# Optimization experiments

Hardware: AMD Instinct MI355X
Metric: run time of the kernel (lower is better)

Reference implementation:

```python
import jax, jax.numpy as jnp
import numpy as np

B, S, H, NH = 8, 1024, 1024, 4
D = H // NH
NEG = jnp.float32(-2**32 + 1)


def setup_inputs() -> dict:
    key = jax.random.key(0)
    ks = jax.random.split(key, 12)
    w = 1.0 / np.sqrt(H)
    wf = 1.0 / np.sqrt(2 * H)
    return {
        "memory": jax.random.normal(ks[0], (B, S, H), jnp.float32),
        "decoder_input": jax.random.normal(ks[1], (B, S, H), jnp.float32),
        "mask": jax.random.bernoulli(ks[2], 0.2, (B, S, S)),
        "query_mask": (jax.random.uniform(ks[3], (B, S)) > 0.1).astype(jnp.float32),
        "Wk": jax.random.normal(ks[4], (H, H), jnp.float32) * w,
        "Wv": jax.random.normal(ks[5], (H, H), jnp.float32) * w,
        "Wq": jax.random.normal(ks[6], (H, H), jnp.float32) * w,
        "Wf": jax.random.normal(ks[7], (2 * H, H), jnp.float32) * wf,
        "bf": jnp.zeros((H,), jnp.float32),
        "gamma": jnp.ones((H,), jnp.float32),
        "beta": jnp.zeros((H,), jnp.float32),
        "g_factor": jax.random.uniform(ks[8], (1,), jnp.float32, 1e4, 2e4),
    }


def reference(memory, decoder_input, mask, query_mask, Wk, Wv, Wq, Wf, bf, gamma, beta, g_factor):
    b, sq, hdim = decoder_input.shape
    sk = memory.shape[1]

    def heads(x, W, s):  # -> (NH, B, s, D), matching torch permute(2,0,1,3)
        return (x @ W).reshape(b, s, NH, D).transpose(2, 0, 1, 3)

    k = heads(memory, Wk, sk)
    v = heads(memory, Wv, sk)
    q = heads(decoder_input, Wq, sq)

    attn = jnp.einsum("hbqd,hbkd->hbqk", q, k) / jnp.sqrt(jnp.float32(D))
    idx = jnp.arange(sk, dtype=jnp.float32)
    gauss = (idx[:, None] - idx[None, :]) ** 2 / g_factor[0]  # (sq, sk), sq==sk
    attn = attn - gauss
    attn = jnp.where(mask[None], NEG, attn)
    attn = jax.nn.softmax(attn, axis=-1)
    attn = attn * query_mask[None, :, :, None]  # post-softmax query mask

    res = jnp.einsum("hbqk,hbkd->hbqd", attn, v)
    res = res.transpose(1, 2, 0, 3).reshape(b, sq, hdim)

    out = jnp.concatenate([decoder_input, res], axis=-1) @ Wf + bf
    out = out + decoder_input
    mu = out.mean(-1, keepdims=True)
    var = ((out - mu) ** 2).mean(-1, keepdims=True)
    out = (out - mu) / jnp.sqrt(var + 1e-5) * gamma + beta
    return out, attn.reshape(NH * b, sq, sk)
```

## Files before the change

### kernel.cpp

```cpp
#include <hip/hip_runtime.h>

#define B_ 8
#define S_ 1024
#define H_ 1024
#define NH_ 4
#define D_ 256
#define M_ 8192

typedef unsigned int u32;
typedef unsigned short u16;
typedef __attribute__((ext_vector_type(4))) float f32x4;
typedef __attribute__((ext_vector_type(8))) short s16x8;

__device__ __forceinline__ float bf2f(u16 b) { return __uint_as_float(((u32)b) << 16); }
__device__ __forceinline__ u16 f2bf(float f) {
    u32 x = __float_as_uint(f);
    return (u16)((x + 0x7fffu + ((x >> 16) & 1u)) >> 16);
}

__global__ void init_flags_k(int* fl) { fl[0] = 0; fl[1] = 0; fl[2] = 0; }

__global__ __launch_bounds__(256) void or_mask_k(const u32* __restrict__ m, int* __restrict__ fl) {
    u32 v = m[blockIdx.x * 256 + threadIdx.x];
#pragma unroll
    for (int o = 32; o; o >>= 1) v |= __shfl_xor(v, o, 64);
    if ((threadIdx.x & 63) == 0) atomicOr(fl + 1, (int)v);
}

__global__ void classify_mask_k(int* fl) {
    u32 R = (u32)fl[1];
    int c;
    if (R == 0x3F803F80u)      c = 2;
    else if (R == 0x3F800000u) c = 3;
    else if (R & 0xFFFFFF00u)  c = 0;
    else                       c = 1;
    fl[2] = c;
}

__global__ __launch_bounds__(256) void tcast_k(const float* __restrict__ src, u16* __restrict__ dst,
                                               int R, int C) {
    __shared__ float sb[32][33];
    const int c0 = blockIdx.x * 32, r0 = blockIdx.y * 32;
    const int tx = threadIdx.x & 31, ty = threadIdx.x >> 5;
#pragma unroll
    for (int i = 0; i < 4; i++)
        sb[ty + 8 * i][tx] = src[(size_t)(r0 + ty + 8 * i) * C + c0 + tx];
    __syncthreads();
#pragma unroll
    for (int i = 0; i < 4; i++)
        dst[(size_t)(c0 + ty + 8 * i) * R + r0 + tx] = f2bf(sb[tx][ty + 8 * i]);
}

__global__ __launch_bounds__(256) void castbf_k(const float* __restrict__ src, u16* __restrict__ dst) {
    const int i = blockIdx.x * 256 + threadIdx.x;
    float4 v = ((const float4*)src)[i];
    ushort4 o;
    o.x = f2bf(v.x); o.y = f2bf(v.y); o.z = f2bf(v.z); o.w = f2bf(v.w);
    ((ushort4*)dst)[i] = o;
}

template<int AMODE>
__device__ __forceinline__ void gemm_core(
    const float* __restrict__ A32, const u16* __restrict__ A16, int lda,
    const u16* __restrict__ Bp, int ldb, int K, int m0, int n0,
    short* As, short* Bs, f32x4 acc[4][4])
{
    const int t = threadIdx.x;
    const int lane = t & 63, wave = t >> 6;
    const int wy = wave >> 1, wx = wave & 1;
    const int mq = lane >> 4, ml = lane & 15;
    const int srow = t >> 2, skq = t & 3;

    for (int k0 = 0; k0 < K; k0 += 32) {
        __syncthreads();
#pragma unroll
        for (int it = 0; it < 2; it++) {
            const int row = srow + it * 64;
            const int kk = k0 + skq * 8;
            short* dst = As + row * 40 + skq * 8;
            if (AMODE == 0) {
                const float* s = A32 + (size_t)(m0 + row) * lda + kk;
                float4 v0 = *(const float4*)s, v1 = *(const float4*)(s + 4);
                s16x8 p;
                p[0] = (short)f2bf(v0.x); p[1] = (short)f2bf(v0.y);
                p[2] = (short)f2bf(v0.z); p[3] = (short)f2bf(v0.w);
                p[4] = (short)f2bf(v1.x); p[5] = (short)f2bf(v1.y);
                p[6] = (short)f2bf(v1.z); p[7] = (short)f2bf(v1.w);
                *(s16x8*)dst = p;
            } else if (AMODE == 1) {
                *(s16x8*)dst = *(const s16x8*)(A16 + (size_t)(m0 + row) * lda + kk);
            } else {
                if (kk < 1024) {
                    const float* s = A32 + (size_t)(m0 + row) * 1024 + kk;
                    float4 v0 = *(const float4*)s, v1 = *(const float4*)(s + 4);
                    s16x8 p;
                    p[0] = (short)f2bf(v0.x); p[1] = (short)f2bf(v0.y);
                    p[2] = (short)f2bf(v0.z); p[3] = (short)f2bf(v0.w);
                    p[4] = (short)f2bf(v1.x); p[5] = (short)f2bf(v1.y);
                    p[6] = (short)f2bf(v1.z); p[7] = (short)f2bf(v1.w);
                    *(s16x8*)dst = p;
                } else {
                    *(s16x8*)dst = *(const s16x8*)(A16 + (size_t)(m0 + row) * 1024 + (kk - 1024));
                }
            }
        }
#pragma unroll
        for (int it = 0; it < 2; it++) {
            const int row = srow + it * 64;
            *(s16x8*)(Bs + row * 40 + skq * 8) =
                *(const s16x8*)(Bp + (size_t)(n0 + row) * ldb + k0 + skq * 8);
        }
        __syncthreads();
        s16x8 af[4], bfr[4];
#pragma unroll
        for (int i = 0; i < 4; i++) {
            af[i]  = *(s16x8*)(As + (wy * 64 + i * 16 + ml) * 40 + mq * 8);
            bfr[i] = *(s16x8*)(Bs + (wx * 64 + i * 16 + ml) * 40 + mq * 8);
        }
#pragma unroll
        for (int mi = 0; mi < 4; mi++)
#pragma unroll
            for (int ni = 0; ni < 4; ni++)
                acc[mi][ni] = __builtin_amdgcn_mfma_f32_16x16x32_bf16(af[mi], bfr[ni], acc[mi][ni], 0, 0, 0);
    }
}

__global__ __launch_bounds__(256) void gemm_proj_k(const u16* __restrict__ A, const u16* __restrict__ WT,
                                                   u16* __restrict__ C) {
    __shared__ short As[128 * 40];
    __shared__ short Bs[128 * 40];
    const int m0 = blockIdx.y * 128, n0 = blockIdx.x * 128;
    f32x4 acc[4][4];
#pragma unroll
    for (int i = 0; i < 4; i++)
#pragma unroll
        for (int j = 0; j < 4; j++) acc[i][j] = 0;
    gemm_core<1>(nullptr, A, H_, WT, H_, H_, m0, n0, As, Bs, acc);
    const int lane = threadIdx.x & 63, wave = threadIdx.x >> 6;
    const int wy = wave >> 1, wx = wave & 1, mq = lane >> 4, ml = lane & 15;
#pragma unroll
    for (int mi = 0; mi < 4; mi++)
#pragma unroll
        for (int ni = 0; ni < 4; ni++) {
            const int n = n0 + wx * 64 + ni * 16 + ml;
#pragma unroll
            for (int r = 0; r < 4; r++) {
                const int m = m0 + wy * 64 + mi * 16 + mq * 4 + r;
                C[(size_t)m * H_ + n] = f2bf(acc[mi][ni][r]);
            }
        }
}

__global__ __launch_bounds__(256) void gemm_vt_k(const u16* __restrict__ A, const u16* __restrict__ WT,
                                                 u16* __restrict__ VT) {
    __shared__ short As[128 * 40];
    __shared__ short Bs[128 * 40];
    const int m0 = blockIdx.y * 128, n0 = blockIdx.x * 128;
    f32x4 acc[4][4];
#pragma unroll
    for (int i = 0; i < 4; i++)
#pragma unroll
        for (int j = 0; j < 4; j++) acc[i][j] = 0;
    gemm_core<1>(nullptr, A, H_, WT, H_, H_, m0, n0, As, Bs, acc);
    const int lane = threadIdx.x & 63, wave = threadIdx.x >> 6;
    const int wy = wave >> 1, wx = wave & 1, mq = lane >> 4, ml = lane & 15;
#pragma unroll
    for (int mi = 0; mi < 4; mi++)
#pragma unroll
        for (int ni = 0; ni < 4; ni++) {
            const int n = n0 + wx * 64 + ni * 16 + ml;
            const int mbase = m0 + wy * 64 + mi * 16 + mq * 4;
            const int b = mbase >> 10, s = mbase & 1023;
            ushort4 w;
            w.x = f2bf(acc[mi][ni][0]); w.y = f2bf(acc[mi][ni][1]);
            w.z = f2bf(acc[mi][ni][2]); w.w = f2bf(acc[mi][ni][3]);
            *(ushort4*)(VT + ((size_t)(b * 1024 + n)) * 1024 + s) = w;
        }
}

__global__ __launch_bounds__(512, 2) void qk_sm_k(
    const u16* __restrict__ Qb, const u16* __restrict__ Kb,
    const void* __restrict__ mask, const float* __restrict__ gfac,
    const int* __restrict__ fl, const float* __restrict__ qmask,
    float* __restrict__ attn)
{
    __shared__ short Bs[1024 * 40];
    __shared__ short As[64 * 40];
    __shared__ float red[2][32][4];

    const int flat = blockIdx.x;
    const int wgid = (flat & 7) * 64 + (flat >> 3);
    const int z = wgid >> 4, m0 = (wgid & 15) * 64;
    const int h = z >> 3, b = z & 7;

    const u16* Aq = Qb + (size_t)b * S_ * H_ + h * D_;
    const u16* Bk = Kb + (size_t)b * S_ * H_ + h * D_;

    const int t = threadIdx.x;
    const int lane = t & 63, wave = t >> 6;
    const int wm = wave >> 2, wn = wave & 3;
    const int mq = lane >> 4, ml = lane & 15;

    f32x4 acc[2][16];
#pragma unroll
    for (int mi = 0; mi < 2; mi++)
#pragma unroll
        for (int nf = 0; nf < 16; nf++) acc[mi][nf] = 0;

    for (int k0 = 0; k0 < D_; k0 += 32) {
        __syncthreads();
        if (t < 256) {
            const int row = t >> 2, kq = t & 3;
            *(s16x8*)(As + row * 40 + kq * 8) =
                *(const s16x8*)(Aq + (size_t)(m0 + row) * H_ + k0 + kq * 8);
        }
#pragma unroll
        for (int it = 0; it < 8; it++) {
            const int c = it * 512 + t;
            const int row = c >> 2, kq = c & 3;
            *(s16x8*)(Bs + row * 40 + kq * 8) =
                *(const s16x8*)(Bk + (size_t)row * H_ + k0 + kq * 8);
        }
        __syncthreads();
        s16x8 af0 = *(s16x8*)(As + (wm * 32 + ml) * 40 + mq * 8);
        s16x8 af1 = *(s16x8*)(As + (wm * 32 + 16 + ml) * 40 + mq * 8);
#pragma unroll
        for (int g4 = 0; g4 < 4; g4++) {
            s16x8 bf4[4];
#pragma unroll
            for (int j = 0; j < 4; j++)
                bf4[j] = *(s16x8*)(Bs + (wn * 256 + (g4 * 4 + j) * 16 + ml) * 40 + mq * 8);
#pragma unroll
            for (int j = 0; j < 4; j++) {
                acc[0][g4 * 4 + j] = __builtin_amdgcn_mfma_f32_16x16x32_bf16(af0, bf4[j], acc[0][g4 * 4 + j], 0, 0, 0);
                acc[1][g4 * 4 + j] = __builtin_amdgcn_mfma_f32_16x16x32_bf16(af1, bf4[j], acc[1][g4 * 4 + j], 0, 0, 0);
            }
        }
    }

    const float ginv = 1.0f / gfac[0];
    const int code = fl[2];
    const size_t zrow = (size_t)z * S_;
    float rmax[2][4], rsum[2][4], scv[2][4];

#pragma unroll
    for (int mi = 0; mi < 2; mi++)
#pragma unroll
        for (int r = 0; r < 4; r++) {
            const int qg = m0 + wm * 32 + mi * 16 + mq * 4 + r;
            const size_t mbase = ((size_t)b * S_ + qg) * S_;
            float mx = -3.0e38f;
#pragma unroll
            for (int nf = 0; nf < 16; nf++) {
                const int kg = wn * 256 + nf * 16 + ml;
                float diff = (float)(qg - kg);
                float val = acc[mi][nf][r] * 0.0625f - diff * diff * ginv;
                int mv;
                if (code == 0)      mv = ((const unsigned char*)mask)[mbase + kg];
                else if (code == 1) mv = ((const int*)mask)[mbase + kg];
                else if (code == 2) mv = (((const u16*)mask)[mbase + kg] != 0);
                else                mv = (((const u32*)mask)[mbase + kg] != 0);
                if (mv) val = -4294967296.0f;
                acc[mi][nf][r] = val;
                mx = fmaxf(mx, val);
            }
            rmax[mi][r] = mx;
        }
#pragma unroll
    for (int o = 1; o < 16; o <<= 1)
#pragma unroll
        for (int mi = 0; mi < 2; mi++)
#pragma unroll
            for (int r = 0; r < 4; r++)
                rmax[mi][r] = fmaxf(rmax[mi][r], __shfl_xor(rmax[mi][r], o, 64));
    if (ml == 0)
#pragma unroll
        for (int mi = 0; mi < 2; mi++)
#pragma unroll
            for (int r = 0; r < 4; r++) red[wm][mi * 16 + mq * 4 + r][wn] = rmax[mi][r];
    __syncthreads();
#pragma unroll
    for (int mi = 0; mi < 2; mi++)
#pragma unroll
        for (int r = 0; r < 4; r++) {
            const int rr = mi * 16 + mq * 4 + r;
            rmax[mi][r] = fmaxf(fmaxf(red[wm][rr][0], red[wm][rr][1]),
                                fmaxf(red[wm][rr][2], red[wm][rr][3]));
        }
    __syncthreads();
#pragma unroll
    for (int mi = 0; mi < 2; mi++)
#pragma unroll
        for (int r = 0; r < 4; r++) {
            float s = 0.f;
#pragma unroll
            for (int nf = 0; nf < 16; nf++) {
                float p = __expf(acc[mi][nf][r] - rmax[mi][r]);
                acc[mi][nf][r] = p;
                s += p;
            }
            rsum[mi][r] = s;
        }
#pragma unroll
    for (int o = 1; o < 16; o <<= 1)
#pragma unroll
        for (int mi = 0; mi < 2; mi++)
#pragma unroll
            for (int r = 0; r < 4; r++) rsum[mi][r] += __shfl_xor(rsum[mi][r], o, 64);
    if (ml == 0)
#pragma unroll
        for (int mi = 0; mi < 2; mi++)
#pragma unroll
            for (int r = 0; r < 4; r++) red[wm][mi * 16 + mq * 4 + r][wn] = rsum[mi][r];
    __syncthreads();
#pragma unroll
    for (int mi = 0; mi < 2; mi++)
#pragma unroll
        for (int r = 0; r < 4; r++) {
            const int rr = mi * 16 + mq * 4 + r;
            const int qg = m0 + wm * 32 + mi * 16 + mq * 4 + r;
            const float s = red[wm][rr][0] + red[wm][rr][1] + red[wm][rr][2] + red[wm][rr][3];
            scv[mi][r] = qmask[b * S_ + qg] / s;
        }
#pragma unroll
    for (int mi = 0; mi < 2; mi++)
#pragma unroll
        for (int r = 0; r < 4; r++) {
            const int qg = m0 + wm * 32 + mi * 16 + mq * 4 + r;
            float* prow = attn + (zrow + qg) * S_ + wn * 256 + ml;
            const float sc = scv[mi][r];
#pragma unroll
            for (int nf = 0; nf < 16; nf++)
                prow[nf * 16] = acc[mi][nf][r] * sc;
        }
}

__global__ __launch_bounds__(256) void pv_mfma_k(const float* __restrict__ attnF, const u16* __restrict__ VT,
                                                 u16* __restrict__ resB) {
    __shared__ short As[128 * 40];
    __shared__ short Bs[128 * 40];
    const int z = blockIdx.z, h = z >> 3, b = z & 7;
    const float* Ap = attnF + (size_t)z * S_ * S_;
    const u16* Bp = VT + ((size_t)(b * 1024 + h * D_)) * 1024;
    const int m0 = blockIdx.y * 128, n0 = blockIdx.x * 128;
    f32x4 acc[4][4];
#pragma unroll
    for (int i = 0; i < 4; i++)
#pragma unroll
        for (int j = 0; j < 4; j++) acc[i][j] = 0;
    gemm_core<0>(Ap, nullptr, S_, Bp, 1024, S_, m0, n0, As, Bs, acc);
    u16* C = resB + (size_t)b * S_ * H_ + h * D_;
    const int lane = threadIdx.x & 63, wave = threadIdx.x >> 6;
    const int wy = wave >> 1, wx = wave & 1, mq = lane >> 4, ml = lane & 15;
#pragma unroll
    for (int mi = 0; mi < 4; mi++)
#pragma unroll
        for (int ni = 0; ni < 4; ni++) {
            const int n = n0 + wx * 64 + ni * 16 + ml;
#pragma unroll
            for (int r = 0; r < 4; r++) {
                const int m = m0 + wy * 64 + mi * 16 + mq * 4 + r;
                C[(size_t)m * H_ + n] = f2bf(acc[mi][ni][r]);
            }
        }
}

__global__ __launch_bounds__(256) void final_mfma_k(const float* __restrict__ dec, const u16* __restrict__ resB,
                                                    const u16* __restrict__ WfT, const float* __restrict__ bfv,
                                                    u16* __restrict__ tmp) {
    __shared__ short As[128 * 40];
    __shared__ short Bs[128 * 40];
    const int m0 = blockIdx.y * 128, n0 = blockIdx.x * 128;
    f32x4 acc[4][4];
#pragma unroll
    for (int i = 0; i < 4; i++)
#pragma unroll
        for (int j = 0; j < 4; j++) acc[i][j] = 0;
    gemm_core<2>(dec, resB, H_, WfT, 2048, 2048, m0, n0, As, Bs, acc);
    const int lane = threadIdx.x & 63, wave = threadIdx.x >> 6;
    const int wy = wave >> 1, wx = wave & 1, mq = lane >> 4, ml = lane & 15;
#pragma unroll
    for (int mi = 0; mi < 4; mi++)
#pragma unroll
        for (int ni = 0; ni < 4; ni++) {
            const int n = n0 + wx * 64 + ni * 16 + ml;
#pragma unroll
            for (int r = 0; r < 4; r++) {
                const int m = m0 + wy * 64 + mi * 16 + mq * 4 + r;
                float val = acc[mi][ni][r] + bfv[n] + dec[(size_t)m * H_ + n];
                tmp[(size_t)m * H_ + n] = f2bf(val);
            }
        }
}

__global__ __launch_bounds__(256) void ln2_k(const u16* __restrict__ tmp, const float* __restrict__ gm,
                                             const float* __restrict__ bt, float* __restrict__ out) {
    const int m = blockIdx.x, t = threadIdx.x;
    ushort4 u = ((const ushort4*)(tmp + (size_t)m * H_))[t];
    float xa[4] = {bf2f(u.x), bf2f(u.y), bf2f(u.z), bf2f(u.w)};
    float s = 0.f, s2 = 0.f;
#pragma unroll
    for (int i = 0; i < 4; i++) { s += xa[i]; s2 += xa[i] * xa[i]; }
#pragma unroll
    for (int o = 32; o; o >>= 1) { s += __shfl_xor(s, o, 64); s2 += __shfl_xor(s2, o, 64); }
    __shared__ float rs[4], rs2[4];
    if ((t & 63) == 0) { rs[t >> 6] = s; rs2[t >> 6] = s2; }
    __syncthreads();
    s  = rs[0] + rs[1] + rs[2] + rs[3];
    s2 = rs2[0] + rs2[1] + rs2[2] + rs2[3];
    float mu = s * (1.f / 1024.f);
    float var = s2 * (1.f / 1024.f) - mu * mu;
    float rstd = rsqrtf(var + 1e-5f);
    float ov[4];
#pragma unroll
    for (int i = 0; i < 4; i++) {
        int n = t * 4 + i;
        ov[i] = (xa[i] - mu) * rstd * gm[n] + bt[n];
    }
    *(float4*)(out + (size_t)m * H_ + t * 4) = make_float4(ov[0], ov[1], ov[2], ov[3]);
}

extern "C" void kernel_launch(void* const* d_in, const int* in_sizes, int n_in,
                              void* d_out, int out_size, void* d_ws, size_t ws_size,
                              hipStream_t stream) {
    const float* memory = (const float*)d_in[0];
    const float* dec    = (const float*)d_in[1];
    const void*  mask   = d_in[2];
    const float* qmask  = (const float*)d_in[3];
    const float* Wk     = (const float*)d_in[4];
    const float* Wv     = (const float*)d_in[5];
    const float* Wq     = (const float*)d_in[6];
    const float* Wf     = (const float*)d_in[7];
    const float* bfv    = (const float*)d_in[8];
    const float* gamma  = (const float*)d_in[9];
    const float* beta   = (const float*)d_in[10];
    const float* gfac   = (const float*)d_in[11];

    char* ws = (char*)d_ws;
    int* fl  = (int*)ws;
    u16* WqT = (u16*)(ws + (1u  << 20));
    u16* WkT = (u16*)(ws + (3u  << 20));
    u16* WvT = (u16*)(ws + (5u  << 20));
    u16* WfT = (u16*)(ws + (7u  << 20));
    u16* Qb  = (u16*)(ws + (11u << 20));
    u16* Kb  = (u16*)(ws + (27u << 20));
    u16* VT  = (u16*)(ws + (43u << 20));
    u16* resB = Kb;
    u16* tmpB = Qb;

    float* out   = (float*)d_out;
    float* attnF = out + (size_t)B_ * S_ * H_;

    u16* memB = (u16*)attnF;
    u16* decB = memB + (size_t)B_ * S_ * H_;

    init_flags_k<<<1, 1, 0, stream>>>(fl);
    or_mask_k<<<256, 256, 0, stream>>>((const u32*)mask, fl);
    classify_mask_k<<<1, 1, 0, stream>>>(fl);

    tcast_k<<<dim3(32, 32), 256, 0, stream>>>(Wq, WqT, 1024, 1024);
    tcast_k<<<dim3(32, 32), 256, 0, stream>>>(Wk, WkT, 1024, 1024);
    tcast_k<<<dim3(32, 32), 256, 0, stream>>>(Wv, WvT, 1024, 1024);
    tcast_k<<<dim3(32, 64), 256, 0, stream>>>(Wf, WfT, 2048, 1024);

    castbf_k<<<8192, 256, 0, stream>>>(memory, memB);
    castbf_k<<<8192, 256, 0, stream>>>(dec,    decB);

    gemm_proj_k<<<dim3(8, 64), 256, 0, stream>>>(decB, WqT, Qb);
    gemm_proj_k<<<dim3(8, 64), 256, 0, stream>>>(memB, WkT, Kb);
    gemm_vt_k  <<<dim3(8, 64), 256, 0, stream>>>(memB, WvT, VT);

    qk_sm_k<<<512, 512, 0, stream>>>(Qb, Kb, mask, gfac, fl, qmask, attnF);
    pv_mfma_k<<<dim3(2, 8, 32), 256, 0, stream>>>(attnF, VT, resB);
    final_mfma_k<<<dim3(8, 64), 256, 0, stream>>>(dec, resB, WfT, bfv, tmpB);
    ln2_k<<<M_, 256, 0, stream>>>(tmpB, gamma, beta, out);
}
```

Measured before the change: 634.2 us.

## Fuse PV matmul into QK-softmax kernel using bf16 probabilities in LDS

After: 616.7 us. 2.8% less time.

```diff
diff --git a/kernel.cpp b/kernel.cpp
--- a/kernel.cpp
+++ b/kernel.cpp
@@ -78,16 +78,7 @@
             const int row = srow + it * 64;
             const int kk = k0 + skq * 8;
             short* dst = As + row * 40 + skq * 8;
-            if (AMODE == 0) {
-                const float* s = A32 + (size_t)(m0 + row) * lda + kk;
-                float4 v0 = *(const float4*)s, v1 = *(const float4*)(s + 4);
-                s16x8 p;
-                p[0] = (short)f2bf(v0.x); p[1] = (short)f2bf(v0.y);
-                p[2] = (short)f2bf(v0.z); p[3] = (short)f2bf(v0.w);
-                p[4] = (short)f2bf(v1.x); p[5] = (short)f2bf(v1.y);
-                p[6] = (short)f2bf(v1.z); p[7] = (short)f2bf(v1.w);
-                *(s16x8*)dst = p;
-            } else if (AMODE == 1) {
+            if (AMODE == 1) {
                 *(s16x8*)dst = *(const s16x8*)(A16 + (size_t)(m0 + row) * lda + kk);
             } else {
                 if (kk < 1024) {
@@ -182,11 +173,14 @@
     const u16* __restrict__ Qb, const u16* __restrict__ Kb,
     const void* __restrict__ mask, const float* __restrict__ gfac,
     const int* __restrict__ fl, const float* __restrict__ qmask,
-    float* __restrict__ attn)
+    float* __restrict__ attn, const u16* __restrict__ VT, u16* __restrict__ resB)
 {
-    __shared__ short Bs[1024 * 40];
-    __shared__ short As[64 * 40];
-    __shared__ float red[2][32][4];
+    __shared__ short smem[76288];
+    short* As = smem;
+    short* Bs = smem + 2560;
+    short* Ps = smem;
+    short* Vs = smem + 65536;
+    float* red = (float*)(smem + 75776);
 
     const int flat = blockIdx.x;
     const int wgid = (flat & 7) * 64 + (flat >> 3);
@@ -277,15 +271,14 @@
 #pragma unroll
         for (int mi = 0; mi < 2; mi++)
 #pragma unroll
-            for (int r = 0; r < 4; r++) red[wm][mi * 16 + mq * 4 + r][wn] = rmax[mi][r];
+            for (int r = 0; r < 4; r++) red[(wm * 32 + mi * 16 + mq * 4 + r) * 4 + wn] = rmax[mi][r];
     __syncthreads();
 #pragma unroll
     for (int mi = 0; mi < 2; mi++)
 #pragma unroll
         for (int r = 0; r < 4; r++) {
-            const int rr = mi * 16 + mq * 4 + r;
-            rmax[mi][r] = fmaxf(fmaxf(red[wm][rr][0], red[wm][rr][1]),
-                                fmaxf(red[wm][rr][2], red[wm][rr][3]));
+            const float* rr = red + (wm * 32 + mi * 16 + mq * 4 + r) * 4;
+            rmax[mi][r] = fmaxf(fmaxf(rr[0], rr[1]), fmaxf(rr[2], rr[3]));
         }
     __syncthreads();
 #pragma unroll
@@ -311,56 +304,77 @@
 #pragma unroll
         for (int mi = 0; mi < 2; mi++)
 #pragma unroll
-            for (int r = 0; r < 4; r++) red[wm][mi * 16 + mq * 4 + r][wn] = rsum[mi][r];
+            for (int r = 0; r < 4; r++) red[(wm * 32 + mi * 16 + mq * 4 + r) * 4 + wn] = rsum[mi][r];
     __syncthreads();
 #pragma unroll
     for (int mi = 0; mi < 2; mi++)
 #pragma unroll
         for (int r = 0; r < 4; r++) {
-            const int rr = mi * 16 + mq * 4 + r;
+            const float* rr = red + (wm * 32 + mi * 16 + mq * 4 + r) * 4;
             const int qg = m0 + wm * 32 + mi * 16 + mq * 4 + r;
-            const float s = red[wm][rr][0] + red[wm][rr][1] + red[wm][rr][2] + red[wm][rr][3];
+            const float s = rr[0] + rr[1] + rr[2] + rr[3];
             scv[mi][r] = qmask[b * S_ + qg] / s;
         }
+
 #pragma unroll
     for (int mi = 0; mi < 2; mi++)
 #pragma unroll
         for (int r = 0; r < 4; r++) {
-            const int qg = m0 + wm * 32 + mi * 16 + mq * 4 + r;
-            float* prow = attn + (zrow + qg) * S_ + wn * 256 + ml;
+            const int prow = wm * 32 + mi * 16 + mq * 4 + r;
+            const int qg = m0 + prow;
+            float* gp = attn + (zrow + qg) * S_ + wn * 256 + ml;
             const float sc = scv[mi][r];
 #pragma unroll
-            for (int nf = 0; nf < 16; nf++)
-                prow[nf * 16] = acc[mi][nf][r] * sc;
-        }
-}
-
-__global__ __launch_bounds__(256) void pv_mfma_k(const float* __restrict__ attnF, const u16* __restrict__ VT,
-                                                 u16* __restrict__ resB) {
-    __shared__ short As[128 * 40];
-    __shared__ short Bs[128 * 40];
-    const int z = blockIdx.z, h = z >> 3, b = z & 7;
-    const float* Ap = attnF + (size_t)z * S_ * S_;
-    const u16* Bp = VT + ((size_t)(b * 1024 + h * D_)) * 1024;
-    const int m0 = blockIdx.y * 128, n0 = blockIdx.x * 128;
-    f32x4 acc[4][4];
-#pragma unroll
-    for (int i = 0; i < 4; i++)
-#pragma unroll
-        for (int j = 0; j < 4; j++) acc[i][j] = 0;
-    gemm_core<0>(Ap, nullptr, S_, Bp, 1024, S_, m0, n0, As, Bs, acc);
+            for (int nf = 0; nf < 16; nf++) {
+                const float v = acc[mi][nf][r] * sc;
+                gp[nf * 16] = v;
+                const int col = wn * 256 + nf * 16 + ml;
+                Ps[prow * 1024 + (col ^ ((prow & 7) << 3))] = (short)f2bf(v);
+            }
+        }
+
+    const int wr = wave >> 2, wc = wave & 3;
+    f32x4 acc2[2][4];
+#pragma unroll
+    for (int mi = 0; mi < 2; mi++)
+#pragma unroll
+        for (int ni = 0; ni < 4; ni++) acc2[mi][ni] = 0;
+
+    const u16* Vp = VT + ((size_t)(b * 1024 + h * D_)) * 1024;
+    for (int k0 = 0; k0 < S_; k0 += 32) {
+        {
+            const int row = t >> 1, half = t & 1;
+            const u16* s = Vp + (size_t)row * 1024 + k0 + half * 16;
+            short* dpt = Vs + row * 40 + half * 16;
+            *(s16x8*)dpt       = *(const s16x8*)s;
+            *(s16x8*)(dpt + 8) = *(const s16x8*)(s + 8);
+        }
+        __syncthreads();
+        s16x8 pa[2];
+#pragma unroll
+        for (int mi = 0; mi < 2; mi++) {
+            const int prow = wr * 32 + mi * 16 + ml;
+            pa[mi] = *(s16x8*)(Ps + prow * 1024 + ((((k0 >> 3) + mq) ^ (prow & 7)) << 3));
+        }
+#pragma unroll
+        for (int ni = 0; ni < 4; ni++) {
+            s16x8 vf = *(s16x8*)(Vs + (wc * 64 + ni * 16 + ml) * 40 + mq * 8);
+            acc2[0][ni] = __builtin_amdgcn_mfma_f32_16x16x32_bf16(pa[0], vf, acc2[0][ni], 0, 0, 0);
+            acc2[1][ni] = __builtin_amdgcn_mfma_f32_16x16x32_bf16(pa[1], vf, acc2[1][ni], 0, 0, 0);
+        }
+        __syncthreads();
+    }
+
     u16* C = resB + (size_t)b * S_ * H_ + h * D_;
-    const int lane = threadIdx.x & 63, wave = threadIdx.x >> 6;
-    const int wy = wave >> 1, wx = wave & 1, mq = lane >> 4, ml = lane & 15;
-#pragma unroll
-    for (int mi = 0; mi < 4; mi++)
+#pragma unroll
+    for (int mi = 0; mi < 2; mi++)
 #pragma unroll
         for (int ni = 0; ni < 4; ni++) {
-            const int n = n0 + wx * 64 + ni * 16 + ml;
+            const int n = wc * 64 + ni * 16 + ml;
 #pragma unroll
             for (int r = 0; r < 4; r++) {
-                const int m = m0 + wy * 64 + mi * 16 + mq * 4 + r;
-                C[(size_t)m * H_ + n] = f2bf(acc[mi][ni][r]);
+                const int m = m0 + wr * 32 + mi * 16 + mq * 4 + r;
+                C[(size_t)m * H_ + n] = f2bf(acc2[mi][ni][r]);
             }
         }
 }
@@ -445,11 +459,12 @@
     u16* Qb  = (u16*)(ws + (11u << 20));
     u16* Kb  = (u16*)(ws + (27u << 20));
     u16* VT  = (u16*)(ws + (43u << 20));
-    u16* resB = Kb;
     u16* tmpB = Qb;
 
     float* out   = (float*)d_out;
     float* attnF = out + (size_t)B_ * S_ * H_;
+
+    u16* resB = (u16*)out;
 
     u16* memB = (u16*)attnF;
     u16* decB = memB + (size_t)B_ * S_ * H_;
@@ -470,8 +485,7 @@
     gemm_proj_k<<<dim3(8, 64), 256, 0, stream>>>(memB, WkT, Kb);
     gemm_vt_k  <<<dim3(8, 64), 256, 0, stream>>>(memB, WvT, VT);
 
-    qk_sm_k<<<512, 512, 0, stream>>>(Qb, Kb, mask, gfac, fl, qmask, attnF);
-    pv_mfma_k<<<dim3(2, 8, 32), 256, 0, stream>>>(attnF, VT, resB);
+    qk_sm_k<<<512, 512, 0, stream>>>(Qb, Kb, mask, gfac, fl, qmask, attnF, VT, resB);
     final_mfma_k<<<dim3(8, 64), 256, 0, stream>>>(dec, resB, WfT, bfv, tmpB);
     ln2_k<<<M_, 256, 0, stream>>>(tmpB, gamma, beta, out);
 }
```
